# Performance work log

Hardware: AMD Instinct MI355X
Metric: run time of the kernel (lower is better)

The kernel has to match this reference:

```python
import jax, jax.numpy as jnp
import numpy as np

EPS = 1e-12

def _l2norm(x):
    return x / jnp.maximum(jnp.linalg.norm(x, axis=-1, keepdims=True), EPS)

def setup_inputs() -> dict:
    key = jax.random.key(0)
    ks = jax.random.split(key, 11)
    B, L, HID, M = 64, 512, 768, 128
    R, P, T = 64, 8, 32
    return {
        "hidden_states": jax.random.normal(ks[0], (B, L, HID), dtype=jnp.float32),
        "ctx_mask": jax.random.randint(ks[1], (B, L), 0, 2, dtype=jnp.int32),
        "between_mask": jax.random.randint(ks[2], (B, L), 0, 2, dtype=jnp.int32),
        "subj_type_id": jax.random.randint(ks[3], (B,), 0, T, dtype=jnp.int32),
        "obj_type_id": jax.random.randint(ks[4], (B,), 0, T, dtype=jnp.int32),
        "subj_first": jax.random.randint(ks[5], (B,), 0, 2, dtype=jnp.int32),
        "proj_W": jax.random.normal(ks[6], (HID, M), dtype=jnp.float32) * 0.02,
        "label_probes": jax.random.normal(ks[7], (R, P, M), dtype=jnp.float32) * 0.02,
        "subj_type_W": jax.random.normal(ks[8], (T, M), dtype=jnp.float32) * 0.02,
        "obj_type_W": jax.random.normal(ks[9], (T, M), dtype=jnp.float32) * 0.02,
        "dir_W": jax.random.normal(ks[10], (2, M), dtype=jnp.float32) * 0.02,
    }

def reference(hidden_states, ctx_mask, between_mask, subj_type_id, obj_type_id,
              subj_first, proj_W, label_probes, subj_type_W, obj_type_W, dir_W):
    # Document token embeddings: project + L2 normalize. [B, L, M]
    D = _l2norm(hidden_states @ proj_W)

    between = between_mask.astype(bool)
    ctx = ctx_mask.astype(bool)
    has_between = jnp.any(between, axis=1)  # [B]
    evidence = jnp.where(has_between[:, None], between, ctx)  # [B, L]

    # Conditioned probes: [B, R, P, M]
    Q = (label_probes[None]
         + subj_type_W[subj_type_id][:, None, None]
         + obj_type_W[obj_type_id][:, None, None]
         + dir_W[subj_first][:, None, None])
    Q = _l2norm(Q)

    # MaxSim: [B, R, P, L]
    sim = jnp.einsum('brhm,blm->brhl', Q, D)
    sim = jnp.where(evidence[:, None, None, :], sim, -10000.0)
    mx = sim.max(axis=3)                        # [B, R, P]
    mx = jnp.where(mx > -1000.0, mx, 0.0)       # zero out fully-masked probes
    logits = mx.sum(axis=2)                     # [B, R]
    return logits
```

## Files before the change

kernel.cpp:

```cpp
#include <hip/hip_runtime.h>
#include <hip/hip_bf16.h>

typedef __attribute__((ext_vector_type(8))) __bf16 bf16x8;
typedef __attribute__((ext_vector_type(4))) float f32x4;

#define B_   64
#define L_   512
#define HID_ 768
#define M_   128
#define R_   64
#define P_   8

__device__ __forceinline__ int swz(int row, int k, int stride) {
    return row * stride + (k ^ ((row & 7) << 3));
}

#define GLL16(gp, lp)                                                        \
    __builtin_amdgcn_global_load_lds(                                        \
        (const __attribute__((address_space(1))) void*)(gp),                 \
        (__attribute__((address_space(3))) void*)(lp), 16, 0, 0)

__global__ __launch_bounds__(256) void k_wt(const float* __restrict__ W,
                                            __bf16* __restrict__ Wt) {
    int idx = blockIdx.x * 256 + threadIdx.x;
    int k = idx >> 7, n = idx & 127;
    int c = k >> 6, kk = k & 63;
    Wt[c * 8192 + n * 64 + (kk ^ ((n & 7) << 3))] = (__bf16)W[idx];
}

__global__ __launch_bounds__(256) void k_proj(const float* __restrict__ hidden,
                                              const __bf16* __restrict__ Wt,
                                              __bf16* __restrict__ D) {
    __shared__ __align__(16) __bf16 Al[2][64 * 64];
    __shared__ __align__(16) __bf16 Bl[2][128 * 64];
    const int t = threadIdx.x;
    const int lane = t & 63, w = t >> 6;
    const int rlo = lane & 15, g = lane >> 4;
    const int row0 = blockIdx.x * 512 + blockIdx.y * 64;

    f32x4 acc[8] = {};

    const int ar = t >> 2;
    const int ac = (t & 3) * 16;
    const float* arow = hidden + (size_t)(row0 + ar) * HID_ + ac;

#pragma unroll
    for (int q = 0; q < 4; ++q)
        GLL16(Wt + q * 2048 + w * 512 + lane * 8, &Bl[0][q * 2048 + w * 512]);
    {
        float4 f0 = ((const float4*)arow)[0];
        float4 f1 = ((const float4*)arow)[1];
        float4 f2 = ((const float4*)arow)[2];
        float4 f3 = ((const float4*)arow)[3];
        bf16x8 v0, v1;
        v0[0]=(__bf16)f0.x; v0[1]=(__bf16)f0.y; v0[2]=(__bf16)f0.z; v0[3]=(__bf16)f0.w;
        v0[4]=(__bf16)f1.x; v0[5]=(__bf16)f1.y; v0[6]=(__bf16)f1.z; v0[7]=(__bf16)f1.w;
        v1[0]=(__bf16)f2.x; v1[1]=(__bf16)f2.y; v1[2]=(__bf16)f2.z; v1[3]=(__bf16)f2.w;
        v1[4]=(__bf16)f3.x; v1[5]=(__bf16)f3.y; v1[6]=(__bf16)f3.z; v1[7]=(__bf16)f3.w;
        *(bf16x8*)&Al[0][swz(ar, ac,     64)] = v0;
        *(bf16x8*)&Al[0][swz(ar, ac + 8, 64)] = v1;
    }
    __syncthreads();

    for (int ci = 0; ci < 12; ++ci) {
        const int cur = ci & 1;
        const bool pre = ci < 11;
        float4 f0, f1, f2, f3;
        if (pre) {
#pragma unroll
            for (int q = 0; q < 4; ++q)
                GLL16(Wt + (ci + 1) * 8192 + q * 2048 + w * 512 + lane * 8,
                      &Bl[cur ^ 1][q * 2048 + w * 512]);
            const float* src = arow + (ci + 1) * 64;
            f0 = ((const float4*)src)[0];
            f1 = ((const float4*)src)[1];
            f2 = ((const float4*)src)[2];
            f3 = ((const float4*)src)[3];
        }
#pragma unroll
        for (int s = 0; s < 2; ++s) {
            int k = s * 32 + g * 8;
            bf16x8 aF = *(const bf16x8*)&Al[cur][swz(w * 16 + rlo, k, 64)];
#pragma unroll
            for (int c = 0; c < 8; ++c) {
                bf16x8 bF = *(const bf16x8*)&Bl[cur][swz(c * 16 + rlo, k, 64)];
                acc[c] = __builtin_amdgcn_mfma_f32_16x16x32_bf16(aF, bF, acc[c], 0, 0, 0);
            }
        }
        if (pre) {
            bf16x8 v0, v1;
            v0[0]=(__bf16)f0.x; v0[1]=(__bf16)f0.y; v0[2]=(__bf16)f0.z; v0[3]=(__bf16)f0.w;
            v0[4]=(__bf16)f1.x; v0[5]=(__bf16)f1.y; v0[6]=(__bf16)f1.z; v0[7]=(__bf16)f1.w;
            v1[0]=(__bf16)f2.x; v1[1]=(__bf16)f2.y; v1[2]=(__bf16)f2.z; v1[3]=(__bf16)f2.w;
            v1[4]=(__bf16)f3.x; v1[5]=(__bf16)f3.y; v1[6]=(__bf16)f3.z; v1[7]=(__bf16)f3.w;
            *(bf16x8*)&Al[cur ^ 1][swz(ar, ac,     64)] = v0;
            *(bf16x8*)&Al[cur ^ 1][swz(ar, ac + 8, 64)] = v1;
        }
        __syncthreads();
    }

    float ss[4] = {0.f, 0.f, 0.f, 0.f};
#pragma unroll
    for (int c = 0; c < 8; ++c)
#pragma unroll
        for (int r = 0; r < 4; ++r) ss[r] += acc[c][r] * acc[c][r];
#pragma unroll
    for (int r = 0; r < 4; ++r)
#pragma unroll
        for (int off = 1; off < 16; off <<= 1) ss[r] += __shfl_xor(ss[r], off);
    float sc[4];
#pragma unroll
    for (int r = 0; r < 4; ++r) sc[r] = 1.0f / fmaxf(sqrtf(ss[r]), 1e-12f);
#pragma unroll
    for (int c = 0; c < 8; ++c)
#pragma unroll
        for (int r = 0; r < 4; ++r) {
            int row = row0 + w * 16 + g * 4 + r;
            int col = c * 16 + rlo;
            D[(size_t)row * M_ + (col ^ ((row & 7) << 3))] = (__bf16)(acc[c][r] * sc[r]);
        }
}

__global__ __launch_bounds__(256) void k_sim(const float* __restrict__ lp,
                                             const float* __restrict__ sW,
                                             const float* __restrict__ oW,
                                             const float* __restrict__ dW,
                                             const int* __restrict__ st,
                                             const int* __restrict__ ot,
                                             const int* __restrict__ sf,
                                             const int* __restrict__ ctx,
                                             const int* __restrict__ btw,
                                             const __bf16* __restrict__ D,
                                             float* __restrict__ out) {
    __shared__ __align__(16) __bf16 Dl[2][128 * 128];
    __shared__ float evl[L_];
    __shared__ int anyf;
    const int t = threadIdx.x;
    const int lane = t & 63, w = t >> 6;
    const int rlo = lane & 15, g = lane >> 4;
    const int b = blockIdx.x, pt = blockIdx.y;

    const __bf16* Db = D + (size_t)b * L_ * M_;

#pragma unroll
    for (int q = 0; q < 8; ++q)
        GLL16(Db + q * 2048 + w * 512 + lane * 8, &Dl[0][q * 2048 + w * 512]);

    if (t == 0) anyf = 0;
    __syncthreads();
    int v0 = btw[b * L_ + t], v1 = btw[b * L_ + t + 256];
    int c0 = ctx[b * L_ + t], c1 = ctx[b * L_ + t + 256];
    if (v0 | v1) anyf = 1;
    __syncthreads();
    const int any = anyf;
    evl[t]       = (any ? v0 : c0) ? 1.0f : 0.0f;
    evl[t + 256] = (any ? v1 : c1) ? 1.0f : 0.0f;

    const int sb = st[b], ob = ot[b], db = sf[b];
    const float* lpp = lp + (size_t)(pt * 64 + w * 16 + rlo) * M_;
    const float* sv  = sW + sb * M_;
    const float* ov  = oW + ob * M_;
    const float* dv  = dW + db * M_;
    float qv[32];
    float ssq = 0.f;
#pragma unroll
    for (int ks = 0; ks < 4; ++ks) {
        const int m0 = ks * 32 + g * 8;
#pragma unroll
        for (int h = 0; h < 2; ++h) {
            float4 a  = *(const float4*)(lpp + m0 + h * 4);
            float4 s4 = *(const float4*)(sv  + m0 + h * 4);
            float4 o4 = *(const float4*)(ov  + m0 + h * 4);
            float4 d4 = *(const float4*)(dv  + m0 + h * 4);
            float x0 = a.x + s4.x + o4.x + d4.x;
            float x1 = a.y + s4.y + o4.y + d4.y;
            float x2 = a.z + s4.z + o4.z + d4.z;
            float x3 = a.w + s4.w + o4.w + d4.w;
            qv[ks * 8 + h * 4 + 0] = x0;
            qv[ks * 8 + h * 4 + 1] = x1;
            qv[ks * 8 + h * 4 + 2] = x2;
            qv[ks * 8 + h * 4 + 3] = x3;
            ssq += x0 * x0 + x1 * x1 + x2 * x2 + x3 * x3;
        }
    }
    ssq += __shfl_xor(ssq, 16);
    ssq += __shfl_xor(ssq, 32);
    const float scq = 1.0f / fmaxf(sqrtf(ssq), 1e-12f);
    bf16x8 qF[4];
#pragma unroll
    for (int ks = 0; ks < 4; ++ks)
#pragma unroll
        for (int j = 0; j < 8; ++j)
            qF[ks][j] = (__bf16)(qv[ks * 8 + j] * scq);

    __syncthreads();

    float vmax[4] = {-1e30f, -1e30f, -1e30f, -1e30f};

    for (int tc = 0; tc < 4; ++tc) {
        const int cur = tc & 1;
        if (tc < 3) {
#pragma unroll
            for (int q = 0; q < 8; ++q)
                GLL16(Db + (tc + 1) * 16384 + q * 2048 + w * 512 + lane * 8,
                      &Dl[cur ^ 1][q * 2048 + w * 512]);
        }
#pragma unroll
        for (int tt = 0; tt < 8; ++tt) {
            f32x4 acc = {};
#pragma unroll
            for (int ks = 0; ks < 4; ++ks) {
                bf16x8 bF = *(const bf16x8*)&Dl[cur][swz(tt * 16 + rlo, ks * 32 + g * 8, 128)];
                acc = __builtin_amdgcn_mfma_f32_16x16x32_bf16(qF[ks], bF, acc, 0, 0, 0);
            }
            float e = evl[tc * 128 + tt * 16 + rlo];
#pragma unroll
            for (int r = 0; r < 4; ++r) {
                float sv2 = (e > 0.5f) ? acc[r] : -1e4f;
                vmax[r] = fmaxf(vmax[r], sv2);
            }
        }
        __syncthreads();
    }

#pragma unroll
    for (int r = 0; r < 4; ++r)
#pragma unroll
        for (int off = 1; off < 16; off <<= 1)
            vmax[r] = fmaxf(vmax[r], __shfl_xor(vmax[r], off));

    float psum = 0.f;
#pragma unroll
    for (int r = 0; r < 4; ++r)
        psum += (vmax[r] > -1000.0f) ? vmax[r] : 0.0f;

    float rtot = psum + __shfl_xor(psum, 16);
    if ((lane & 31) == 0) {
        int rr = pt * 8 + w * 2 + (g >> 1);
        out[b * R_ + rr] = rtot;
    }
}

extern "C" void kernel_launch(void* const* d_in, const int* in_sizes, int n_in,
                              void* d_out, int out_size, void* d_ws, size_t ws_size,
                              hipStream_t stream) {
    const float* hidden = (const float*)d_in[0];
    const int*   ctx    = (const int*)d_in[1];
    const int*   btw    = (const int*)d_in[2];
    const int*   st     = (const int*)d_in[3];
    const int*   ot     = (const int*)d_in[4];
    const int*   sf     = (const int*)d_in[5];
    const float* W      = (const float*)d_in[6];
    const float* lp     = (const float*)d_in[7];
    const float* sW     = (const float*)d_in[8];
    const float* oW     = (const float*)d_in[9];
    const float* dW     = (const float*)d_in[10];
    float* out = (float*)d_out;

    char* ws = (char*)d_ws;
    __bf16* Wt = (__bf16*)ws;
    __bf16* D  = (__bf16*)(ws + 196608);

    k_wt  <<<(HID_ * M_) / 256, 256, 0, stream>>>(W, Wt);
    k_proj<<<dim3(B_, 8), 256, 0, stream>>>(hidden, Wt, D);
    k_sim <<<dim3(B_, 8), 256, 0, stream>>>(lp, sW, oW, dW, st, ot, sf, ctx, btw, D, out);
}
```

Baseline: 46.08 us.

## Split projection GEMM columns across 8 waves and stage output through LDS

The projection kernel now launches 512 threads per block, with waves split into 4 row blocks by 2 column halves, so each wave holds 4 accumulators instead of 8. The row-norm reduction crosses the two column halves through a small shared buffer and an extra barrier. The normalized tile is written into LDS and then stored to global memory as coalesced 16-byte vectors instead of scattered 2-byte stores. The aim is more latency hiding and better store efficiency, at the cost of extra barriers and fewer loads in flight per thread.

```diff
diff --git a/kernel.cpp b/kernel.cpp
--- a/kernel.cpp
+++ b/kernel.cpp
@@ -28,97 +28,105 @@
     Wt[c * 8192 + n * 64 + (kk ^ ((n & 7) << 3))] = (__bf16)W[idx];
 }
 
-__global__ __launch_bounds__(256) void k_proj(const float* __restrict__ hidden,
-                                              const __bf16* __restrict__ Wt,
-                                              __bf16* __restrict__ D) {
+__global__ __launch_bounds__(512, 4) void k_proj(const float* __restrict__ hidden,
+                                                 const __bf16* __restrict__ Wt,
+                                                 __bf16* __restrict__ D) {
     __shared__ __align__(16) __bf16 Al[2][64 * 64];
     __shared__ __align__(16) __bf16 Bl[2][128 * 64];
+    __shared__ float nbuf[2][64];
     const int t = threadIdx.x;
     const int lane = t & 63, w = t >> 6;
     const int rlo = lane & 15, g = lane >> 4;
+    const int rb = w & 3, ch = w >> 2;
     const int row0 = blockIdx.x * 512 + blockIdx.y * 64;
 
-    f32x4 acc[8] = {};
-
-    const int ar = t >> 2;
-    const int ac = (t & 3) * 16;
+    f32x4 acc[4] = {};
+
+    const int ar = t >> 3;
+    const int ac = (t & 7) * 8;
     const float* arow = hidden + (size_t)(row0 + ar) * HID_ + ac;
 
-#pragma unroll
-    for (int q = 0; q < 4; ++q)
-        GLL16(Wt + q * 2048 + w * 512 + lane * 8, &Bl[0][q * 2048 + w * 512]);
+    GLL16(Wt + w * 1024 + lane * 8,       &Bl[0][w * 1024]);
+    GLL16(Wt + w * 1024 + 512 + lane * 8, &Bl[0][w * 1024 + 512]);
     {
-        float4 f0 = ((const float4*)arow)[0];
-        float4 f1 = ((const float4*)arow)[1];
-        float4 f2 = ((const float4*)arow)[2];
-        float4 f3 = ((const float4*)arow)[3];
-        bf16x8 v0, v1;
-        v0[0]=(__bf16)f0.x; v0[1]=(__bf16)f0.y; v0[2]=(__bf16)f0.z; v0[3]=(__bf16)f0.w;
-        v0[4]=(__bf16)f1.x; v0[5]=(__bf16)f1.y; v0[6]=(__bf16)f1.z; v0[7]=(__bf16)f1.w;
-        v1[0]=(__bf16)f2.x; v1[1]=(__bf16)f2.y; v1[2]=(__bf16)f2.z; v1[3]=(__bf16)f2.w;
-        v1[4]=(__bf16)f3.x; v1[5]=(__bf16)f3.y; v1[6]=(__bf16)f3.z; v1[7]=(__bf16)f3.w;
-        *(bf16x8*)&Al[0][swz(ar, ac,     64)] = v0;
-        *(bf16x8*)&Al[0][swz(ar, ac + 8, 64)] = v1;
+        float4 f0 = *(const float4*)(arow);
+        float4 f1 = *(const float4*)(arow + 4);
+        bf16x8 v;
+        v[0]=(__bf16)f0.x; v[1]=(__bf16)f0.y; v[2]=(__bf16)f0.z; v[3]=(__bf16)f0.w;
+        v[4]=(__bf16)f1.x; v[5]=(__bf16)f1.y; v[6]=(__bf16)f1.z; v[7]=(__bf16)f1.w;
+        *(bf16x8*)&Al[0][swz(ar, ac, 64)] = v;
     }
     __syncthreads();
 
     for (int ci = 0; ci < 12; ++ci) {
         const int cur = ci & 1;
         const bool pre = ci < 11;
-        float4 f0, f1, f2, f3;
+        float4 f0, f1;
         if (pre) {
-#pragma unroll
-            for (int q = 0; q < 4; ++q)
-                GLL16(Wt + (ci + 1) * 8192 + q * 2048 + w * 512 + lane * 8,
-                      &Bl[cur ^ 1][q * 2048 + w * 512]);
+            const __bf16* wsrc = Wt + (ci + 1) * 8192 + w * 1024;
+            GLL16(wsrc + lane * 8,       &Bl[cur ^ 1][w * 1024]);
+            GLL16(wsrc + 512 + lane * 8, &Bl[cur ^ 1][w * 1024 + 512]);
             const float* src = arow + (ci + 1) * 64;
-            f0 = ((const float4*)src)[0];
-            f1 = ((const float4*)src)[1];
-            f2 = ((const float4*)src)[2];
-            f3 = ((const float4*)src)[3];
+            f0 = *(const float4*)(src);
+            f1 = *(const float4*)(src + 4);
         }
 #pragma unroll
         for (int s = 0; s < 2; ++s) {
-            int k = s * 32 + g * 8;
-            bf16x8 aF = *(const bf16x8*)&Al[cur][swz(w * 16 + rlo, k, 64)];
-#pragma unroll
-            for (int c = 0; c < 8; ++c) {
-                bf16x8 bF = *(const bf16x8*)&Bl[cur][swz(c * 16 + rlo, k, 64)];
+            int kk = s * 32 + g * 8;
+            bf16x8 aF = *(const bf16x8*)&Al[cur][swz(rb * 16 + rlo, kk, 64)];
+#pragma unroll
+            for (int c = 0; c < 4; ++c) {
+                bf16x8 bF = *(const bf16x8*)&Bl[cur][swz(ch * 64 + c * 16 + rlo, kk, 64)];
                 acc[c] = __builtin_amdgcn_mfma_f32_16x16x32_bf16(aF, bF, acc[c], 0, 0, 0);
             }
         }
         if (pre) {
-            bf16x8 v0, v1;
-            v0[0]=(__bf16)f0.x; v0[1]=(__bf16)f0.y; v0[2]=(__bf16)f0.z; v0[3]=(__bf16)f0.w;
-            v0[4]=(__bf16)f1.x; v0[5]=(__bf16)f1.y; v0[6]=(__bf16)f1.z; v0[7]=(__bf16)f1.w;
-            v1[0]=(__bf16)f2.x; v1[1]=(__bf16)f2.y; v1[2]=(__bf16)f2.z; v1[3]=(__bf16)f2.w;
-            v1[4]=(__bf16)f3.x; v1[5]=(__bf16)f3.y; v1[6]=(__bf16)f3.z; v1[7]=(__bf16)f3.w;
-            *(bf16x8*)&Al[cur ^ 1][swz(ar, ac,     64)] = v0;
-            *(bf16x8*)&Al[cur ^ 1][swz(ar, ac + 8, 64)] = v1;
+            bf16x8 v;
+            v[0]=(__bf16)f0.x; v[1]=(__bf16)f0.y; v[2]=(__bf16)f0.z; v[3]=(__bf16)f0.w;
+            v[4]=(__bf16)f1.x; v[5]=(__bf16)f1.y; v[6]=(__bf16)f1.z; v[7]=(__bf16)f1.w;
+            *(bf16x8*)&Al[cur ^ 1][swz(ar, ac, 64)] = v;
         }
         __syncthreads();
     }
 
     float ss[4] = {0.f, 0.f, 0.f, 0.f};
 #pragma unroll
-    for (int c = 0; c < 8; ++c)
+    for (int c = 0; c < 4; ++c)
 #pragma unroll
         for (int r = 0; r < 4; ++r) ss[r] += acc[c][r] * acc[c][r];
 #pragma unroll
     for (int r = 0; r < 4; ++r)
 #pragma unroll
         for (int off = 1; off < 16; off <<= 1) ss[r] += __shfl_xor(ss[r], off);
+    if (rlo == 0) {
+#pragma unroll
+        for (int r = 0; r < 4; ++r) nbuf[ch][rb * 16 + g * 4 + r] = ss[r];
+    }
+    __syncthreads();
     float sc[4];
 #pragma unroll
-    for (int r = 0; r < 4; ++r) sc[r] = 1.0f / fmaxf(sqrtf(ss[r]), 1e-12f);
-#pragma unroll
-    for (int c = 0; c < 8; ++c)
+    for (int r = 0; r < 4; ++r) {
+        float tot = nbuf[0][rb * 16 + g * 4 + r] + nbuf[1][rb * 16 + g * 4 + r];
+        sc[r] = 1.0f / fmaxf(sqrtf(tot), 1e-12f);
+    }
+
+    __bf16* Dst = (__bf16*)Al;
+#pragma unroll
+    for (int c = 0; c < 4; ++c)
 #pragma unroll
         for (int r = 0; r < 4; ++r) {
-            int row = row0 + w * 16 + g * 4 + r;
-            int col = c * 16 + rlo;
-            D[(size_t)row * M_ + (col ^ ((row & 7) << 3))] = (__bf16)(acc[c][r] * sc[r]);
-        }
+            int row = rb * 16 + g * 4 + r;
+            int col = ch * 64 + c * 16 + rlo;
+            Dst[row * 128 + (col ^ ((row & 7) << 3))] = (__bf16)(acc[c][r] * sc[r]);
+        }
+    __syncthreads();
+#pragma unroll
+    for (int h = 0; h < 2; ++h) {
+        int row = (t >> 4) + h * 32;
+        int seg = t & 15;
+        bf16x8 v = *(const bf16x8*)&Dst[row * 128 + seg * 8];
+        *(bf16x8*)(D + (size_t)(row0 + row) * M_ + seg * 8) = v;
+    }
 }
 
 __global__ __launch_bounds__(256) void k_sim(const float* __restrict__ lp,
@@ -262,6 +270,6 @@
     __bf16* D  = (__bf16*)(ws + 196608);
 
     k_wt  <<<(HID_ * M_) / 256, 256, 0, stream>>>(W, Wt);
-    k_proj<<<dim3(B_, 8), 256, 0, stream>>>(hidden, Wt, D);
+    k_proj<<<dim3(B_, 8), 512, 0, stream>>>(hidden, Wt, D);
     k_sim <<<dim3(B_, 8), 256, 0, stream>>>(lp, sW, oW, dW, st, ot, sf, ctx, btw, D, out);
 }
```

New measurement: 44.01 us. 4.5% less time.
